# Kernel tuning notes

Hardware: AMD Instinct MI355X
Metric: run time of the kernel (lower is better)

Reference implementation:

```python
import jax, jax.numpy as jnp
import numpy as np

B, T, F, H, S = 32, 2000, 80, 256, 100
CH = [256, 256]
D = 2 * H  # bidirectional output dim


def _conv1d_relu(x, w, b):
    # x: (B,C_in,T), w: (C_out,C_in,3), 'same' padding, eval-mode dropout = identity
    y = jax.lax.conv_general_dilated(x, w, (1,), [(1, 1)], dimension_numbers=("NCH", "OIH", "NCH"))
    return jax.nn.relu(y + b[None, :, None])


def _lstm_dir(x, mask, wih, whh, b):
    # Masked LSTM == packed-sequence semantics: state frozen and output zero past length.
    # PyTorch gate order: i, f, g, o.  x: (B,T,I), mask: (B,T) bool
    Bb = x.shape[0]
    Hh = whh.shape[1]
    h0 = jnp.zeros((Bb, Hh), x.dtype)

    def step(carry, inp):
        h, c = carry
        xt, mt = inp
        g = xt @ wih.T + h @ whh.T + b
        i, f, gg, o = jnp.split(g, 4, axis=-1)
        i = jax.nn.sigmoid(i)
        f = jax.nn.sigmoid(f)
        gg = jnp.tanh(gg)
        o = jax.nn.sigmoid(o)
        cn = f * c + i * gg
        hn = o * jnp.tanh(cn)
        m = mt[:, None]
        return (jnp.where(m, hn, h), jnp.where(m, cn, c)), jnp.where(m, hn, 0.0)

    _, ys = jax.lax.scan(step, (h0, h0), (jnp.swapaxes(x, 0, 1), jnp.swapaxes(mask, 0, 1)))
    return jnp.swapaxes(ys, 0, 1)  # (B,T,H)


def _bilstm_layer(x, mask, lengths, wih, whh, b):
    fwd = _lstm_dir(x, mask, wih[0], whh[0], b[0])
    t = jnp.arange(x.shape[1])[None, :]
    # reverse each sequence within its valid prefix (involution), identity on padding
    rev_idx = jnp.where(t < lengths[:, None], lengths[:, None] - 1 - t, t)
    x_rev = jnp.take_along_axis(x, rev_idx[:, :, None], axis=1)
    bwd = _lstm_dir(x_rev, mask, wih[1], whh[1], b[1])
    bwd = jnp.take_along_axis(bwd, rev_idx[:, :, None], axis=1)
    return jnp.concatenate([fwd, bwd], axis=-1)


def _head(x, w1, b1, w2, b2):
    # Linear -> ReLU -> (Dropout=id) -> Linear(.,1), squeeze last dim
    return (jax.nn.relu(x @ w1.T + b1) @ w2.T + b2)[..., 0]


def _forward(features, feat_lengths, phoneme_segments, seg_lengths,
             conv1_w, conv1_b, conv2_w, conv2_b,
             wih0, whh0, bias0, wih1, whh1, bias1,
             seg_w1, seg_b1, seg_w2, seg_b2,
             utt_w1, utt_b1, utt_w2, utt_b2):
    x = jnp.swapaxes(features, 1, 2)  # (B,F,T)
    x = _conv1d_relu(x, conv1_w, conv1_b)
    x = _conv1d_relu(x, conv2_w, conv2_b)
    x = jnp.swapaxes(x, 1, 2)  # (B,T,C)

    t = jnp.arange(x.shape[1])[None, :]
    mask = t < feat_lengths[:, None]  # (B,T)

    h = _bilstm_layer(x, mask, feat_lengths, wih0, whh0, bias0)
    lstm_out = _bilstm_layer(h, mask, feat_lengths, wih1, whh1, bias1)  # (B,T,2H), zeros at pads

    denom = jnp.maximum(feat_lengths, 1).astype(lstm_out.dtype)[:, None]
    pooled = lstm_out.sum(axis=1) / denom
    utterance_score = _head(pooled, utt_w1, utt_b1, utt_w2, utt_b2)  # (B,)

    # vectorized segment mean-pool (replaces the python double loop)
    s = jnp.clip(phoneme_segments[..., 0], 0, feat_lengths[:, None])
    e = jnp.maximum(s + 1, jnp.minimum(phoneme_segments[..., 1], feat_lengths[:, None]))
    seg_mask = (t[:, None, :] >= s[..., None]) & (t[:, None, :] < e[..., None])  # (B,S,T)
    counts = (e - s).astype(lstm_out.dtype)
    seg_mean = jnp.einsum("bst,btd->bsd", seg_mask.astype(lstm_out.dtype), lstm_out) / counts[..., None]
    scores = _head(seg_mean, seg_w1, seg_b1, seg_w2, seg_b2)  # (B,S)
    valid = jnp.arange(scores.shape[1])[None, :] < seg_lengths[:, None]
    phoneme_scores = jnp.where(valid, scores, 0.0)
    return utterance_score, phoneme_scores


def setup_inputs() -> dict:
    key = jax.random.key(0)
    ks = jax.random.split(key, 24)
    sc = 0.05
    features = jax.random.normal(ks[0], (B, T, F), jnp.float32)
    feat_lengths = jax.random.randint(ks[1], (B,), T // 2, T + 1, dtype=jnp.int32)
    sidx = jnp.arange(S, dtype=jnp.int32)
    starts = (feat_lengths[:, None] * sidx) // S
    ends = (feat_lengths[:, None] * (sidx + 1)) // S
    phoneme_segments = jnp.stack([starts, ends], axis=-1).astype(jnp.int32)  # (B,S,2)
    seg_lengths = jnp.full((B,), S, dtype=jnp.int32)
    return {
        "features": features,
        "feat_lengths": feat_lengths,
        "phoneme_segments": phoneme_segments,
        "seg_lengths": seg_lengths,
        "conv1_w": jax.random.normal(ks[2], (CH[0], F, 3), jnp.float32) * sc,
        "conv1_b": jnp.zeros((CH[0],), jnp.float32),
        "conv2_w": jax.random.normal(ks[3], (CH[1], CH[0], 3), jnp.float32) * sc,
        "conv2_b": jnp.zeros((CH[1],), jnp.float32),
        "wih0": jax.random.normal(ks[4], (2, 4 * H, CH[1]), jnp.float32) * sc,
        "whh0": jax.random.normal(ks[5], (2, 4 * H, H), jnp.float32) * sc,
        "bias0": jnp.zeros((2, 4 * H), jnp.float32),
        "wih1": jax.random.normal(ks[6], (2, 4 * H, 2 * H), jnp.float32) * sc,
        "whh1": jax.random.normal(ks[7], (2, 4 * H, H), jnp.float32) * sc,
        "bias1": jnp.zeros((2, 4 * H), jnp.float32),
        "seg_w1": jax.random.normal(ks[8], (D, D), jnp.float32) * sc,
        "seg_b1": jnp.zeros((D,), jnp.float32),
        "seg_w2": jax.random.normal(ks[9], (1, D), jnp.float32) * sc,
        "seg_b2": jnp.zeros((1,), jnp.float32),
        "utt_w1": jax.random.normal(ks[10], (D, D), jnp.float32) * sc,
        "utt_b1": jnp.zeros((D,), jnp.float32),
        "utt_w2": jax.random.normal(ks[11], (1, D), jnp.float32) * sc,
        "utt_b2": jnp.zeros((1,), jnp.float32),
    }


def reference(features, feat_lengths, phoneme_segments, seg_lengths,
              conv1_w, conv1_b, conv2_w, conv2_b,
              wih0, whh0, bias0, wih1, whh1, bias1,
              seg_w1, seg_b1, seg_w2, seg_b2,
              utt_w1, utt_b1, utt_w2, utt_b2):
    return _forward(features, feat_lengths, phoneme_segments, seg_lengths,
                    conv1_w, conv1_b, conv2_w, conv2_b,
                    wih0, whh0, bias0, wih1, whh1, bias1,
                    seg_w1, seg_b1, seg_w2, seg_b2,
                    utt_w1, utt_b1, utt_w2, utt_b2)
```

## Files before the change

### kernel.cpp

```cpp
#include <hip/hip_runtime.h>
#include <math.h>

#define T_SEQ 2000
#define BATCH 32
#define NSEG  100

typedef unsigned short bf16_t;
typedef unsigned int   u32;
typedef _Float16       half_t;
typedef half_t half2_t __attribute__((ext_vector_type(2)));

#define KP_REG 96
#define KP_LDS 32
#define NG     (KP_LDS / 4)

#define REC_BAR() do {                                         \
    __builtin_amdgcn_sched_barrier(0);                         \
    asm volatile("s_waitcnt lgkmcnt(0)" ::: "memory");         \
    __builtin_amdgcn_s_barrier();                              \
    __builtin_amdgcn_sched_barrier(0);                         \
} while (0)

__device__ __forceinline__ float sigmoidf_(float x) {
    return 1.0f / (1.0f + __expf(-x));
}
__device__ __forceinline__ float tanh_(float x) {
    return 1.0f - 2.0f / (__expf(2.0f * x) + 1.0f);
}
__device__ __forceinline__ float bf2f(bf16_t u) {
    return __uint_as_float((unsigned)u << 16);
}
__device__ __forceinline__ bf16_t f2bf(float f) {
    unsigned x = __float_as_uint(f);
    return (bf16_t)((x + 0x7FFFu + ((x >> 16) & 1u)) >> 16);
}
__device__ __forceinline__ u32 f2h(float f) {
    return (u32)__builtin_bit_cast(unsigned short, (half_t)f);
}
__device__ __forceinline__ float dot2f(u32 w, u32 h, float acc) {
    return __builtin_amdgcn_fdot2(__builtin_bit_cast(half2_t, w),
                                  __builtin_bit_cast(half2_t, h), acc, false);
}
__device__ __forceinline__ u32 rl(u32 v, int l) {
    return (u32)__builtin_amdgcn_readlane((int)v, l);
}

__device__ __forceinline__ float4 ld4(const float* p) { return *(const float4*)p; }
__device__ __forceinline__ float4 ld4(const bf16_t* p) {
    ushort4 u = *(const ushort4*)p;
    return make_float4(bf2f(u.x), bf2f(u.y), bf2f(u.z), bf2f(u.w));
}

__global__ void ws_guard_kernel(float* out, int n) {
    int i = blockIdx.x * blockDim.x + threadIdx.x;
    if (i < n) out[i] = 1e30f;
}

__global__ void transpose3(const float* __restrict__ in, float* __restrict__ out,
                           int D0, int D1, int D2) {
    int i = blockIdx.x * blockDim.x + threadIdx.x;
    int tot = D0 * D1 * D2;
    if (i >= tot) return;
    int d0 = i / (D1 * D2);
    int r  = i - d0 * (D1 * D2);
    int d1 = r / D2;
    int d2 = r - d1 * D2;
    out[(size_t)d0 * D1 * D2 + (size_t)d2 * D1 + d1] = in[i];
}

__global__ __launch_bounds__(256) void pack_whh(const float* __restrict__ whhT,
                                                u32* __restrict__ w16,
                                                u32* __restrict__ wp4) {
    int i = blockIdx.x * 256 + threadIdx.x;
    int d  = i >> 17;
    int r  = i & 131071;
    int kp = r >> 10;
    int j  = r & 1023;
    const float* base = whhT + (size_t)d * 262144;
    u32 lo = f2h(base[(size_t)(2 * kp)     * 1024 + j]);
    u32 hi = f2h(base[(size_t)(2 * kp + 1) * 1024 + j]);
    u32 val = lo | (hi << 16);
    w16[i] = val;
    if (kp >= KP_REG) {
        int g  = (kp - KP_REG) >> 2;
        int cc = (kp - KP_REG) & 3;
        size_t idx = ((((size_t)d * 2 + (j & 1)) * NG + g) * 512 + (j >> 1)) * 4 + cc;
        wp4[idx] = val;
    }
}

template <int MODE, int CIN, typename TA, bool OUT_BF>
__global__ __launch_bounds__(256) void gemm_nt(
    const TA* __restrict__ A, const float* __restrict__ W,
    const float* __restrict__ bias, void* __restrict__ Cout,
    void* __restrict__ Cout2,
    int M, int N, int K, int relu, int t0, int chunkM,
    const int* __restrict__ lens)
{
    __shared__ u32 As[16 * 258];
    __shared__ u32 Ws[16 * 66];
    const int tid    = threadIdx.x;
    const int m_base = blockIdx.x * 256;
    const int n_base = blockIdx.y * 64;
    const int m0     = (tid >> 3) * 8;
    const int n0     = (tid & 7) * 8;
    int zrev = 0;
    if constexpr (MODE == 4) {
        zrev = blockIdx.z;
        if (zrev) { W += (size_t)N * K; bias += N; Cout = Cout2; }
    }
    float acc[8][8] = {};

    for (int k0 = 0; k0 < K; k0 += 32) {
#pragma unroll
        for (int i = 0; i < 8; ++i) {
            int f4  = i * 256 + tid;
            int row = f4 >> 3;
            int k4  = (f4 & 7) << 2;
            int gm  = m_base + row;
            int gk  = k0 + k4;
            float4 v = make_float4(0.f, 0.f, 0.f, 0.f);
            if (gm < M && gk < K) {
                if constexpr (MODE == 1) {
                    int bb  = gm / T_SEQ;
                    int tt  = gm - bb * T_SEQ;
                    int tap = gk / CIN;
                    int cc  = gk - tap * CIN;
                    int ts  = tt + tap - 1;
                    if (ts >= 0 && ts < T_SEQ)
                        v = ld4(A + ((size_t)(bb * T_SEQ + ts) * CIN + cc));
                } else {
                    int bb = gm / chunkM;
                    int r  = gm - bb * chunkM;
                    int t  = zrev ? (lens[bb] - 1 - (t0 + r)) : (t0 + r);
                    if (t >= 0 && t < T_SEQ)
                        v = ld4(A + ((size_t)(bb * T_SEQ + t) * K + gk));
                }
            }
            int kp = k4 >> 1;
            As[(kp + 0) * 258 + row] = f2h(v.x) | (f2h(v.y) << 16);
            As[(kp + 1) * 258 + row] = f2h(v.z) | (f2h(v.w) << 16);
        }
#pragma unroll
        for (int i = 0; i < 2; ++i) {
            int f4  = i * 256 + tid;
            int row = f4 >> 3;
            int k4  = (f4 & 7) << 2;
            int gn  = n_base + row;
            int gk  = k0 + k4;
            float4 v = make_float4(0.f, 0.f, 0.f, 0.f);
            if (gk < K)
                v = *(const float4*)(W + (size_t)gn * K + gk);
            int kp = k4 >> 1;
            Ws[(kp + 0) * 66 + row] = f2h(v.x) | (f2h(v.y) << 16);
            Ws[(kp + 1) * 66 + row] = f2h(v.z) | (f2h(v.w) << 16);
        }
        __syncthreads();
#pragma unroll 8
        for (int kk = 0; kk < 16; ++kk) {
            u32 am[8], wn[8];
#pragma unroll
            for (int j = 0; j < 4; ++j) {
                uint2 a = *(const uint2*)(As + kk * 258 + m0 + 2 * j);
                am[2 * j] = a.x; am[2 * j + 1] = a.y;
                uint2 w = *(const uint2*)(Ws + kk * 66 + n0 + 2 * j);
                wn[2 * j] = w.x; wn[2 * j + 1] = w.y;
            }
#pragma unroll
            for (int im = 0; im < 8; ++im)
#pragma unroll
                for (int in = 0; in < 8; ++in)
                    acc[im][in] = dot2f(am[im], wn[in], acc[im][in]);
        }
        __syncthreads();
    }

    float bs[8];
#pragma unroll
    for (int j = 0; j < 8; ++j) bs[j] = bias[n_base + n0 + j];
#pragma unroll
    for (int im = 0; im < 8; ++im) {
        int gm = m_base + m0 + im;
        if (gm < M) {
            float o[8];
#pragma unroll
            for (int j = 0; j < 8; ++j) {
                float v = acc[im][j] + bs[j];
                o[j] = relu ? fmaxf(v, 0.f) : v;
            }
            if constexpr (OUT_BF) {
                bf16_t* crow = (bf16_t*)Cout + (size_t)gm * N + n_base + n0;
                ushort4 u0 = { f2bf(o[0]), f2bf(o[1]), f2bf(o[2]), f2bf(o[3]) };
                ushort4 u1 = { f2bf(o[4]), f2bf(o[5]), f2bf(o[6]), f2bf(o[7]) };
                *(ushort4*)(crow)     = u0;
                *(ushort4*)(crow + 4) = u1;
            } else {
                float* crow = (float*)Cout + (size_t)gm * N + n_base + n0;
                *(float4*)(crow)     = make_float4(o[0], o[1], o[2], o[3]);
                *(float4*)(crow + 4) = make_float4(o[4], o[5], o[6], o[7]);
            }
        }
    }
}

__global__
__attribute__((amdgpu_flat_work_group_size(512, 512), amdgpu_waves_per_eu(2, 2)))
void rec_fused(
    const float* __restrict__ XpF, const float* __restrict__ XpB,
    const u32* __restrict__ whh16, const uint4* __restrict__ wp4,
    const int* __restrict__ lens,
    float* __restrict__ state, bf16_t* __restrict__ Hout, int s0, int chunk,
    const bf16_t* __restrict__ Ag, const float* __restrict__ Wg2,
    const float* __restrict__ biasg, float* __restrict__ XpFn,
    float* __restrict__ XpBn, int Kg, int t0n)
{
    __shared__ __align__(16) u32 smem[32768 + 1024 + 128];

    const int t = threadIdx.x;

    if (blockIdx.x < 64) {
        uint4* wlds4 = (uint4*)smem;
        float* gs    = (float*)(smem + 32768);
        u32*   hp    = smem + 32768 + 1024;

        const int bd   = blockIdx.x;
        const int b    = bd >> 1;
        const int d    = bd & 1;
        const int j0   = t * 2;
        const int lane = t & 63;
        const int len  = lens[b];
        const int s1   = min(s0 + chunk, len);
        const u32*   Wg = whh16 + (size_t)d * (128 * 1024);
        const uint4* Wp = wp4   + (size_t)d * (2 * NG * 512);

        uint2 w2[KP_REG];
#pragma unroll
        for (int kp = 0; kp < KP_REG; ++kp)
            w2[kp] = *(const uint2*)(Wg + (size_t)kp * 1024 + j0);
#pragma unroll
        for (int i = 0; i < 2 * NG; ++i)
            wlds4[i * 512 + t] = Wp[i * 512 + t];

        float* st = state + bd * 512;
        float c = 0.f, hcur = 0.f;
        if (t < 256) {
            if (s0 > 0) { hcur = st[t]; c = st[256 + t]; }
            u32 hb = f2h(hcur);
            u32 ob = (u32)__shfl_xor((int)hb, 1);
            if (!(t & 1)) hp[t >> 1] = hb | (ob << 16);
        }
        __syncthreads();

        const float* xrow = ((d ? XpB : XpF) + (size_t)b * ((size_t)chunk * 1024));
        const uint4* wpA = wlds4 + t;
        const uint4* wpB = wlds4 + NG * 512 + t;
        for (int s = s0; s < s1; ++s, xrow += 1024) {
            float2 xv = *(const float2*)(xrow + j0);
            uint2 hreg = *(const uint2*)(hp + 2 * lane);
            float a0 = 0.f, a1 = 0.f, b0 = 0.f, b1 = 0.f;
#pragma unroll
            for (int kp = 0; kp < KP_REG; kp += 2) {
                u32 h0 = rl(hreg.x, kp >> 1);
                u32 h1 = rl(hreg.y, kp >> 1);
                a0 = dot2f(w2[kp].x,     h0, a0); a1 = dot2f(w2[kp].y,     h0, a1);
                b0 = dot2f(w2[kp + 1].x, h1, b0); b1 = dot2f(w2[kp + 1].y, h1, b1);
            }
#pragma unroll
            for (int g = 0; g < NG; ++g) {
                uint4 wA = wpA[g * 512];
                uint4 wB = wpB[g * 512];
                const int lb = (KP_REG >> 1) + 2 * g;
                u32 h0 = rl(hreg.x, lb);
                u32 h1 = rl(hreg.y, lb);
                u32 h2 = rl(hreg.x, lb + 1);
                u32 h3 = rl(hreg.y, lb + 1);
                a0 = dot2f(wA.x, h0, a0); a1 = dot2f(wB.x, h0, a1);
                b0 = dot2f(wA.y, h1, b0); b1 = dot2f(wB.y, h1, b1);
                a0 = dot2f(wA.z, h2, a0); a1 = dot2f(wB.z, h2, a1);
                b0 = dot2f(wA.w, h3, b0); b1 = dot2f(wB.w, h3, b1);
            }
            *(float2*)(gs + j0) = make_float2(a0 + b0 + xv.x, a1 + b1 + xv.y);
            REC_BAR();
            if (t < 256) {
                float ig = sigmoidf_(gs[t]);
                float fg = sigmoidf_(gs[256 + t]);
                float gg = tanh_(gs[512 + t]);
                float og = sigmoidf_(gs[768 + t]);
                c = fmaf(fg, c, ig * gg);
                float hn = og * tanh_(c);
                const int tau = d ? (len - 1 - s) : s;
                Hout[(size_t)(b * T_SEQ + tau) * 512 + (d << 8) + t] = f2bf(hn);
                u32 hb = f2h(hn);
                u32 ob = (u32)__shfl_xor((int)hb, 1);
                if (!(t & 1)) hp[t >> 1] = hb | (ob << 16);
                hcur = hn;
            }
            REC_BAR();
        }
        if (t < 256) { st[t] = hcur; st[256 + t] = c; }
        return;
    }

    if (t0n < 0) return;
    const int ngb = gridDim.x - 64;
    const int gb  = blockIdx.x - 64;
    u32* As  = smem;
    u32* Ws0 = smem + 4128;
    u32* Ws1 = smem + 4128 + 1056;
    const int half = t >> 8;
    const int ltid = t & 255;
    u32* Wsh = half ? Ws1 : Ws0;
    const int m0  = (ltid >> 3) * 8;
    const int n0l = (ltid & 7) * 8;
    const int Mc  = 32 * chunk;
    const int gxm = (Mc + 255) >> 8;
    const int U   = gxm * 8 * 2;

    for (int u = gb; u < U; u += ngb) {
        const int dir  = u & 1;
        const int rem  = u >> 1;
        const int mt   = rem >> 3;
        const int np   = rem & 7;
        const int m_base = mt * 256;
        const int n_base = np * 128 + half * 64;
        const float* Wd = Wg2 + (size_t)dir * (1024 * (size_t)Kg);
        const float* bd = biasg + dir * 1024;
        float* Xout = dir ? XpBn : XpFn;
        float acc[8][8] = {};

        for (int k0 = 0; k0 < Kg; k0 += 32) {
#pragma unroll
            for (int i = 0; i < 4; ++i) {
                int f4  = i * 512 + t;
                int row = f4 >> 3;
                int k4  = (f4 & 7) << 2;
                int gm  = m_base + row;
                int gk  = k0 + k4;
                float4 v = make_float4(0.f, 0.f, 0.f, 0.f);
                if (gm < Mc && gk < Kg) {
                    int bb = gm / chunk;
                    int rr = gm - bb * chunk;
                    int tt = dir ? (lens[bb] - 1 - (t0n + rr)) : (t0n + rr);
                    if (tt >= 0 && tt < T_SEQ)
                        v = ld4(Ag + ((size_t)(bb * T_SEQ + tt) * Kg + gk));
                }
                int kp = k4 >> 1;
                As[(kp + 0) * 258 + row] = f2h(v.x) | (f2h(v.y) << 16);
                As[(kp + 1) * 258 + row] = f2h(v.z) | (f2h(v.w) << 16);
            }
#pragma unroll
            for (int i = 0; i < 2; ++i) {
                int f4  = i * 256 + ltid;
                int row = f4 >> 3;
                int k4  = (f4 & 7) << 2;
                int gn  = n_base + row;
                int gk  = k0 + k4;
                float4 v = make_float4(0.f, 0.f, 0.f, 0.f);
                if (gk < Kg)
                    v = *(const float4*)(Wd + (size_t)gn * Kg + gk);
                int kp = k4 >> 1;
                Wsh[(kp + 0) * 66 + row] = f2h(v.x) | (f2h(v.y) << 16);
                Wsh[(kp + 1) * 66 + row] = f2h(v.z) | (f2h(v.w) << 16);
            }
            __syncthreads();
#pragma unroll 8
            for (int kk = 0; kk < 16; ++kk) {
                u32 am[8], wn[8];
#pragma unroll
                for (int j = 0; j < 4; ++j) {
                    uint2 a = *(const uint2*)(As + kk * 258 + m0 + 2 * j);
                    am[2 * j] = a.x; am[2 * j + 1] = a.y;
                    uint2 w = *(const uint2*)(Wsh + kk * 66 + n0l + 2 * j);
                    wn[2 * j] = w.x; wn[2 * j + 1] = w.y;
                }
#pragma unroll
                for (int im = 0; im < 8; ++im)
#pragma unroll
                    for (int in = 0; in < 8; ++in)
                        acc[im][in] = dot2f(am[im], wn[in], acc[im][in]);
            }
            __syncthreads();
        }

        float bs[8];
#pragma unroll
        for (int j = 0; j < 8; ++j) bs[j] = bd[n_base + n0l + j];
#pragma unroll
        for (int im = 0; im < 8; ++im) {
            int gm = m_base + m0 + im;
            if (gm < Mc) {
                float* crow = Xout + (size_t)gm * 1024 + n_base + n0l;
                *(float4*)(crow)     = make_float4(acc[im][0] + bs[0], acc[im][1] + bs[1],
                                                   acc[im][2] + bs[2], acc[im][3] + bs[3]);
                *(float4*)(crow + 4) = make_float4(acc[im][4] + bs[4], acc[im][5] + bs[5],
                                                   acc[im][6] + bs[6], acc[im][7] + bs[7]);
            }
        }
    }
}

__global__ __launch_bounds__(256) void pooled_kernel(
    const bf16_t* __restrict__ L, const int* __restrict__ lens,
    float* __restrict__ pooled)
{
    const int b     = blockIdx.x;
    const int chunk = blockIdx.y;
    const int tid   = threadIdx.x;
    const int len   = lens[b];
    const int t0    = chunk * 250;
    const int t1    = min(t0 + 250, len);
    const float inv = 1.f / fmaxf((float)len, 1.f);
    float s0 = 0.f, s1 = 0.f;
    for (int t = t0; t < t1; ++t) {
        const bf16_t* row = L + (size_t)(b * T_SEQ + t) * 512;
        s0 += bf2f(row[tid]);
        s1 += bf2f(row[tid + 256]);
    }
    if (t1 > t0) {
        atomicAdd(&pooled[b * 512 + tid], s0 * inv);
        atomicAdd(&pooled[b * 512 + 256 + tid], s1 * inv);
    }
}

__global__ __launch_bounds__(256) void utt_head(
    const float* __restrict__ pooled,
    const float* __restrict__ w1T, const float* __restrict__ b1,
    const float* __restrict__ w2, const float* __restrict__ b2,
    float* __restrict__ out)
{
    const int b   = blockIdx.x;
    const int tid = threadIdx.x;
    __shared__ float p[512];
    __shared__ float hid[512];
    __shared__ float red[4];
    p[tid]       = pooled[b * 512 + tid];
    p[tid + 256] = pooled[b * 512 + 256 + tid];
    __syncthreads();
#pragma unroll
    for (int half = 0; half < 2; ++half) {
        int u = tid + half * 256;
        float a = b1[u];
#pragma unroll 8
        for (int k = 0; k < 512; ++k) a = fmaf(w1T[(size_t)k * 512 + u], p[k], a);
        hid[u] = fmaxf(a, 0.f);
    }
    __syncthreads();
    float part = hid[tid] * w2[tid] + hid[tid + 256] * w2[tid + 256];
    for (int off = 32; off; off >>= 1) part += __shfl_down(part, off, 64);
    if ((tid & 63) == 0) red[tid >> 6] = part;
    __syncthreads();
    if (tid == 0) out[b] = red[0] + red[1] + red[2] + red[3] + b2[0];
}

__global__ __launch_bounds__(256) void seg_head(
    const bf16_t* __restrict__ L, const int* __restrict__ lens,
    const int* __restrict__ segs,
    const float* __restrict__ w1T, const float* __restrict__ b1,
    const float* __restrict__ w2, const float* __restrict__ b2,
    const int* __restrict__ seg_lens, float* __restrict__ out)
{
    const int blk = blockIdx.x;
    const int b   = blk / NSEG;
    const int s   = blk - b * NSEG;
    const int tid = threadIdx.x;
    __shared__ float m[512];
    __shared__ float hid[512];
    __shared__ float red[4];
    const int len = lens[b];
    int st = segs[blk * 2 + 0];
    int en = segs[blk * 2 + 1];
    st = min(max(st, 0), len);
    en = max(st + 1, min(en, len));
    const float inv = 1.f / (float)(en - st);
    float a0 = 0.f, a1 = 0.f;
    for (int t = st; t < en; ++t) {
        const bf16_t* row = L + (size_t)(b * T_SEQ + t) * 512;
        a0 += bf2f(row[tid]);
        a1 += bf2f(row[tid + 256]);
    }
    m[tid]       = a0 * inv;
    m[tid + 256] = a1 * inv;
    __syncthreads();
#pragma unroll
    for (int half = 0; half < 2; ++half) {
        int u = tid + half * 256;
        float a = b1[u];
#pragma unroll 8
        for (int k = 0; k < 512; ++k) a = fmaf(w1T[(size_t)k * 512 + u], m[k], a);
        hid[u] = fmaxf(a, 0.f);
    }
    __syncthreads();
    float part = hid[tid] * w2[tid] + hid[tid + 256] * w2[tid + 256];
    for (int off = 32; off; off >>= 1) part += __shfl_down(part, off, 64);
    if ((tid & 63) == 0) red[tid >> 6] = part;
    __syncthreads();
    if (tid == 0)
        out[BATCH + blk] = (s < seg_lens[b]) ? red[0] + red[1] + red[2] + red[3] + b2[0]
                                             : 0.f;
}

extern "C" void kernel_launch(void* const* d_in, const int* in_sizes, int n_in,
                              void* d_out, int out_size, void* d_ws, size_t ws_size,
                              hipStream_t stream)
{
    const float* features = (const float*)d_in[0];
    const int*   feat_len = (const int*)d_in[1];
    const int*   segs     = (const int*)d_in[2];
    const int*   seg_lens = (const int*)d_in[3];
    const float* conv1_w  = (const float*)d_in[4];
    const float* conv1_b  = (const float*)d_in[5];
    const float* conv2_w  = (const float*)d_in[6];
    const float* conv2_b  = (const float*)d_in[7];
    const float* wih0     = (const float*)d_in[8];
    const float* whh0     = (const float*)d_in[9];
    const float* bias0    = (const float*)d_in[10];
    const float* wih1     = (const float*)d_in[11];
    const float* whh1     = (const float*)d_in[12];
    const float* bias1    = (const float*)d_in[13];
    const float* seg_w1   = (const float*)d_in[14];
    const float* seg_b1   = (const float*)d_in[15];
    const float* seg_w2   = (const float*)d_in[16];
    const float* seg_b2   = (const float*)d_in[17];
    const float* utt_w1   = (const float*)d_in[18];
    const float* utt_b1   = (const float*)d_in[19];
    const float* utt_w2   = (const float*)d_in[20];
    const float* utt_b2   = (const float*)d_in[21];
    float* out = (float*)d_out;
    char*  wsb = (char*)d_ws;

    size_t off = 0;
    auto alloc = [&](size_t bytes) -> size_t {
        size_t o = off;
        off += (bytes + 255) & ~(size_t)255;
        return o;
    };
    const size_t o_wt1    = alloc(61440  * 4);
    const size_t o_wt2    = alloc(196608 * 4);
    const size_t o_whh0T  = alloc(524288 * 4);
    const size_t o_whh1T  = alloc(524288 * 4);
    const size_t o_w16_0  = alloc(262144 * 4);
    const size_t o_w16_1  = alloc(262144 * 4);
    const size_t o_wp4_0  = alloc((size_t)2 * 2 * NG * 512 * 16);
    const size_t o_wp4_1  = alloc((size_t)2 * 2 * NG * 512 * 16);
    const size_t o_sw1T   = alloc(262144 * 4);
    const size_t o_uw1T   = alloc(262144 * 4);
    const size_t o_state  = alloc(32768  * 4);
    const size_t o_pooled = alloc(16384  * 4);
    const size_t o_Hcat   = alloc((size_t)32768000 * 2);
    const size_t o_lstm   = alloc((size_t)32768000 * 2);
    const size_t o_y1     = o_lstm;
    const size_t o_x2     = o_lstm + (size_t)16384000 * 2;
    const size_t fixed_end = off;

    const int cands[] = {250, 200, 125, 100, 50, 40, 25, 20, 10};
    int chunk = 0;
    size_t o_Xp[2][2] = {};
    for (int ci = 0; ci < 9; ++ci) {
        int c = cands[ci];
        size_t xp_bytes = ((size_t)c * 32 * 1024 * 4 + 255) & ~(size_t)255;
        if (fixed_end + 4 * xp_bytes <= ws_size) {
            chunk = c;
            o_Xp[0][0] = fixed_end;
            o_Xp[0][1] = fixed_end + xp_bytes;
            o_Xp[1][0] = fixed_end + 2 * xp_bytes;
            o_Xp[1][1] = fixed_end + 3 * xp_bytes;
            break;
        }
    }
    if (chunk == 0) {
        ws_guard_kernel<<<(out_size + 255) / 256, 256, 0, stream>>>(out, out_size);
        return;
    }
    const int nph = T_SEQ / chunk;

    float*  wt1    = (float*)(wsb + o_wt1);
    float*  wt2    = (float*)(wsb + o_wt2);
    float*  whh0T  = (float*)(wsb + o_whh0T);
    float*  whh1T  = (float*)(wsb + o_whh1T);
    u32*    w16_0  = (u32*)(wsb + o_w16_0);
    u32*    w16_1  = (u32*)(wsb + o_w16_1);
    u32*    wp4_0  = (u32*)(wsb + o_wp4_0);
    u32*    wp4_1  = (u32*)(wsb + o_wp4_1);
    float*  sw1T   = (float*)(wsb + o_sw1T);
    float*  uw1T   = (float*)(wsb + o_uw1T);
    float*  state  = (float*)(wsb + o_state);
    float*  pooled = (float*)(wsb + o_pooled);
    bf16_t* Hcat   = (bf16_t*)(wsb + o_Hcat);
    bf16_t* lstm   = (bf16_t*)(wsb + o_lstm);
    bf16_t* y1     = (bf16_t*)(wsb + o_y1);
    bf16_t* x2     = (bf16_t*)(wsb + o_x2);
    float*  XpF[2] = { (float*)(wsb + o_Xp[0][0]), (float*)(wsb + o_Xp[1][0]) };
    float*  XpB[2] = { (float*)(wsb + o_Xp[0][1]), (float*)(wsb + o_Xp[1][1]) };

    hipMemsetAsync(state, 0, 32768 * 4, stream);
    hipMemsetAsync(pooled, 0, 16384 * 4, stream);

    transpose3<<<240, 256, 0, stream>>>(conv1_w, wt1, 256, 80, 3);
    transpose3<<<768, 256, 0, stream>>>(conv2_w, wt2, 256, 256, 3);
    transpose3<<<2048, 256, 0, stream>>>(whh0, whh0T, 2, 1024, 256);
    transpose3<<<2048, 256, 0, stream>>>(whh1, whh1T, 2, 1024, 256);
    transpose3<<<1024, 256, 0, stream>>>(seg_w1, sw1T, 1, 512, 512);
    transpose3<<<1024, 256, 0, stream>>>(utt_w1, uw1T, 1, 512, 512);
    pack_whh<<<1024, 256, 0, stream>>>(whh0T, w16_0, wp4_0);
    pack_whh<<<1024, 256, 0, stream>>>(whh1T, w16_1, wp4_1);

    gemm_nt<1, 80, float, true><<<dim3(250, 4), 256, 0, stream>>>(
        features, wt1, conv1_b, y1, nullptr, 64000, 256, 240, 1, 0, 0, feat_len);
    gemm_nt<1, 256, bf16_t, true><<<dim3(250, 4), 256, 0, stream>>>(
        y1, wt2, conv2_b, x2, nullptr, 64000, 256, 768, 1, 0, 0, feat_len);

    const int gx = (32 * chunk + 255) / 256;
    const int Mc = 32 * chunk;

    gemm_nt<4, 1, bf16_t, false><<<dim3(gx, 16, 2), 256, 0, stream>>>(
        x2, wih0, bias0, XpF[0], XpB[0], Mc, 1024, 256, 0, 0, chunk, feat_len);
    for (int p = 0; p < nph; ++p) {
        const int t0n = (p + 1 < nph) ? (p + 1) * chunk : -1;
        rec_fused<<<256, 512, 0, stream>>>(
            XpF[p & 1], XpB[p & 1], w16_0, (const uint4*)wp4_0, feat_len,
            state, Hcat, p * chunk, chunk,
            x2, wih0, bias0, XpF[(p + 1) & 1], XpB[(p + 1) & 1], 256, t0n);
    }

    hipMemsetAsync(state, 0, 32768 * 4, stream);

    gemm_nt<4, 1, bf16_t, false><<<dim3(gx, 16, 2), 256, 0, stream>>>(
        Hcat, wih1, bias1, XpF[0], XpB[0], Mc, 1024, 512, 0, 0, chunk, feat_len);
    for (int p = 0; p < nph; ++p) {
        const int t0n = (p + 1 < nph) ? (p + 1) * chunk : -1;
        rec_fused<<<256, 512, 0, stream>>>(
            XpF[p & 1], XpB[p & 1], w16_1, (const uint4*)wp4_1, feat_len,
            state, lstm, p * chunk, chunk,
            Hcat, wih1, bias1, XpF[(p + 1) & 1], XpB[(p + 1) & 1], 512, t0n);
    }

    pooled_kernel<<<dim3(32, 8), 256, 0, stream>>>(lstm, feat_len, pooled);
    utt_head<<<32, 256, 0, stream>>>(pooled, uw1T, utt_b1, utt_w2, utt_b2, out);

    seg_head<<<3200, 256, 0, stream>>>(lstm, feat_len, segs, sw1T, seg_b1,
                                       seg_w2, seg_b2, seg_lens, out);
}
```

Measured before the change: 8.667 ms.

## Halve recurrent block to 256 threads, each computing four gate columns

The recurrent LSTM kernel moves from 512 to 256 threads per block, and each thread now produces four gate outputs instead of two. More of W_hh is held in registers (104 of 128 k-pairs), and the rest sits in a repacked LDS layout. This shrinks the per-step barrier and gate-nonlinearity overhead, since every thread is now active in the elementwise phase. The cost is much higher register pressure at one wave per EU, a risk of spills, and half the threads on the overlapped input-projection GEMM blocks, which are reworked to a single 64-wide N tile.

```diff
diff --git a/kernel.cpp b/kernel.cpp
--- a/kernel.cpp
+++ b/kernel.cpp
@@ -10,9 +10,8 @@
 typedef _Float16       half_t;
 typedef half_t half2_t __attribute__((ext_vector_type(2)));
 
-#define KP_REG 96
-#define KP_LDS 32
-#define NG     (KP_LDS / 4)
+#define KP_REG 104
+#define KP_LDS 24
 
 #define REC_BAR() do {                                         \
     __builtin_amdgcn_sched_barrier(0);                         \
@@ -82,9 +81,8 @@
     u32 val = lo | (hi << 16);
     w16[i] = val;
     if (kp >= KP_REG) {
-        int g  = (kp - KP_REG) >> 2;
-        int cc = (kp - KP_REG) & 3;
-        size_t idx = ((((size_t)d * 2 + (j & 1)) * NG + g) * 512 + (j >> 1)) * 4 + cc;
+        int kpl = kp - KP_REG;
+        size_t idx = (((size_t)d * KP_LDS + kpl) * 256 + (j >> 2)) * 4 + (j & 3);
         wp4[idx] = val;
     }
 }
@@ -204,7 +202,7 @@
 }
 
 __global__
-__attribute__((amdgpu_flat_work_group_size(512, 512), amdgpu_waves_per_eu(2, 2)))
+__attribute__((amdgpu_flat_work_group_size(256, 256), amdgpu_waves_per_eu(1, 1)))
 void rec_fused(
     const float* __restrict__ XpF, const float* __restrict__ XpB,
     const u32* __restrict__ whh16, const uint4* __restrict__ wp4,
@@ -214,37 +212,37 @@
     const float* __restrict__ biasg, float* __restrict__ XpFn,
     float* __restrict__ XpBn, int Kg, int t0n)
 {
-    __shared__ __align__(16) u32 smem[32768 + 1024 + 128];
+    __shared__ __align__(16) u32 smem[KP_LDS * 1024 + 1024 + 128];
 
     const int t = threadIdx.x;
 
     if (blockIdx.x < 64) {
         uint4* wlds4 = (uint4*)smem;
-        float* gs    = (float*)(smem + 32768);
-        u32*   hp    = smem + 32768 + 1024;
+        float* gs    = (float*)(smem + KP_LDS * 1024);
+        u32*   hp    = smem + KP_LDS * 1024 + 1024;
 
         const int bd   = blockIdx.x;
         const int b    = bd >> 1;
         const int d    = bd & 1;
-        const int j0   = t * 2;
+        const int j0   = t * 4;
         const int lane = t & 63;
         const int len  = lens[b];
         const int s1   = min(s0 + chunk, len);
         const u32*   Wg = whh16 + (size_t)d * (128 * 1024);
-        const uint4* Wp = wp4   + (size_t)d * (2 * NG * 512);
-
-        uint2 w2[KP_REG];
+        const uint4* Wp = wp4   + (size_t)d * (KP_LDS * 256);
+
+        uint4 w4[KP_REG];
 #pragma unroll
         for (int kp = 0; kp < KP_REG; ++kp)
-            w2[kp] = *(const uint2*)(Wg + (size_t)kp * 1024 + j0);
-#pragma unroll
-        for (int i = 0; i < 2 * NG; ++i)
-            wlds4[i * 512 + t] = Wp[i * 512 + t];
+            w4[kp] = *(const uint4*)(Wg + (size_t)kp * 1024 + j0);
+#pragma unroll
+        for (int i = 0; i < KP_LDS; ++i)
+            wlds4[i * 256 + t] = Wp[i * 256 + t];
 
         float* st = state + bd * 512;
         float c = 0.f, hcur = 0.f;
-        if (t < 256) {
-            if (s0 > 0) { hcur = st[t]; c = st[256 + t]; }
+        if (s0 > 0) { hcur = st[t]; c = st[256 + t]; }
+        {
             u32 hb = f2h(hcur);
             u32 ob = (u32)__shfl_xor((int)hb, 1);
             if (!(t & 1)) hp[t >> 1] = hb | (ob << 16);
@@ -252,36 +250,38 @@
         __syncthreads();
 
         const float* xrow = ((d ? XpB : XpF) + (size_t)b * ((size_t)chunk * 1024));
-        const uint4* wpA = wlds4 + t;
-        const uint4* wpB = wlds4 + NG * 512 + t;
+        const uint4* wpT = wlds4 + t;
         for (int s = s0; s < s1; ++s, xrow += 1024) {
-            float2 xv = *(const float2*)(xrow + j0);
+            float4 xv = *(const float4*)(xrow + j0);
             uint2 hreg = *(const uint2*)(hp + 2 * lane);
-            float a0 = 0.f, a1 = 0.f, b0 = 0.f, b1 = 0.f;
+            float e0 = 0.f, e1 = 0.f, e2 = 0.f, e3 = 0.f;
+            float o0 = 0.f, o1 = 0.f, o2 = 0.f, o3 = 0.f;
 #pragma unroll
             for (int kp = 0; kp < KP_REG; kp += 2) {
                 u32 h0 = rl(hreg.x, kp >> 1);
                 u32 h1 = rl(hreg.y, kp >> 1);
-                a0 = dot2f(w2[kp].x,     h0, a0); a1 = dot2f(w2[kp].y,     h0, a1);
-                b0 = dot2f(w2[kp + 1].x, h1, b0); b1 = dot2f(w2[kp + 1].y, h1, b1);
-            }
-#pragma unroll
-            for (int g = 0; g < NG; ++g) {
-                uint4 wA = wpA[g * 512];
-                uint4 wB = wpB[g * 512];
-                const int lb = (KP_REG >> 1) + 2 * g;
-                u32 h0 = rl(hreg.x, lb);
-                u32 h1 = rl(hreg.y, lb);
-                u32 h2 = rl(hreg.x, lb + 1);
-                u32 h3 = rl(hreg.y, lb + 1);
-                a0 = dot2f(wA.x, h0, a0); a1 = dot2f(wB.x, h0, a1);
-                b0 = dot2f(wA.y, h1, b0); b1 = dot2f(wB.y, h1, b1);
-                a0 = dot2f(wA.z, h2, a0); a1 = dot2f(wB.z, h2, a1);
-                b0 = dot2f(wA.w, h3, b0); b1 = dot2f(wB.w, h3, b1);
-            }
-            *(float2*)(gs + j0) = make_float2(a0 + b0 + xv.x, a1 + b1 + xv.y);
+                uint4 vE = w4[kp], vO = w4[kp + 1];
+                e0 = dot2f(vE.x, h0, e0); e1 = dot2f(vE.y, h0, e1);
+                e2 = dot2f(vE.z, h0, e2); e3 = dot2f(vE.w, h0, e3);
+                o0 = dot2f(vO.x, h1, o0); o1 = dot2f(vO.y, h1, o1);
+                o2 = dot2f(vO.z, h1, o2); o3 = dot2f(vO.w, h1, o3);
+            }
+#pragma unroll
+            for (int kpl = 0; kpl < KP_LDS; kpl += 2) {
+                uint4 vE = wpT[(kpl + 0) * 256];
+                uint4 vO = wpT[(kpl + 1) * 256];
+                const int pi = (KP_REG >> 1) + (kpl >> 1);
+                u32 h0 = rl(hreg.x, pi);
+                u32 h1 = rl(hreg.y, pi);
+                e0 = dot2f(vE.x, h0, e0); e1 = dot2f(vE.y, h0, e1);
+                e2 = dot2f(vE.z, h0, e2); e3 = dot2f(vE.w, h0, e3);
+                o0 = dot2f(vO.x, h1, o0); o1 = dot2f(vO.y, h1, o1);
+                o2 = dot2f(vO.z, h1, o2); o3 = dot2f(vO.w, h1, o3);
+            }
+            *(float4*)(gs + j0) = make_float4(e0 + o0 + xv.x, e1 + o1 + xv.y,
+                                              e2 + o2 + xv.z, e3 + o3 + xv.w);
             REC_BAR();
-            if (t < 256) {
+            {
                 float ig = sigmoidf_(gs[t]);
                 float fg = sigmoidf_(gs[256 + t]);
                 float gg = tanh_(gs[512 + t]);
@@ -297,32 +297,29 @@
             }
             REC_BAR();
         }
-        if (t < 256) { st[t] = hcur; st[256 + t] = c; }
+        st[t] = hcur;
+        st[256 + t] = c;
         return;
     }
 
     if (t0n < 0) return;
     const int ngb = gridDim.x - 64;
     const int gb  = blockIdx.x - 64;
-    u32* As  = smem;
-    u32* Ws0 = smem + 4128;
-    u32* Ws1 = smem + 4128 + 1056;
-    const int half = t >> 8;
-    const int ltid = t & 255;
-    u32* Wsh = half ? Ws1 : Ws0;
-    const int m0  = (ltid >> 3) * 8;
-    const int n0l = (ltid & 7) * 8;
+    u32* As = smem;
+    u32* Ws = smem + 4128;
+    const int m0 = (t >> 3) * 8;
+    const int n0 = (t & 7) * 8;
     const int Mc  = 32 * chunk;
     const int gxm = (Mc + 255) >> 8;
-    const int U   = gxm * 8 * 2;
+    const int U   = gxm * 16 * 2;
 
     for (int u = gb; u < U; u += ngb) {
-        const int dir  = u & 1;
-        const int rem  = u >> 1;
-        const int mt   = rem >> 3;
-        const int np   = rem & 7;
+        const int dir = u & 1;
+        const int rem = u >> 1;
+        const int mt  = rem >> 4;
+        const int nt  = rem & 15;
         const int m_base = mt * 256;
-        const int n_base = np * 128 + half * 64;
+        const int n_base = nt * 64;
         const float* Wd = Wg2 + (size_t)dir * (1024 * (size_t)Kg);
         const float* bd = biasg + dir * 1024;
         float* Xout = dir ? XpBn : XpFn;
@@ -330,8 +327,8 @@
 
         for (int k0 = 0; k0 < Kg; k0 += 32) {
 #pragma unroll
-            for (int i = 0; i < 4; ++i) {
-                int f4  = i * 512 + t;
+            for (int i = 0; i < 8; ++i) {
+                int f4  = i * 256 + t;
                 int row = f4 >> 3;
                 int k4  = (f4 & 7) << 2;
                 int gm  = m_base + row;
@@ -350,7 +347,7 @@
             }
 #pragma unroll
             for (int i = 0; i < 2; ++i) {
-                int f4  = i * 256 + ltid;
+                int f4  = i * 256 + t;
                 int row = f4 >> 3;
                 int k4  = (f4 & 7) << 2;
                 int gn  = n_base + row;
@@ -359,8 +356,8 @@
                 if (gk < Kg)
                     v = *(const float4*)(Wd + (size_t)gn * Kg + gk);
                 int kp = k4 >> 1;
-                Wsh[(kp + 0) * 66 + row] = f2h(v.x) | (f2h(v.y) << 16);
-                Wsh[(kp + 1) * 66 + row] = f2h(v.z) | (f2h(v.w) << 16);
+                Ws[(kp + 0) * 66 + row] = f2h(v.x) | (f2h(v.y) << 16);
+                Ws[(kp + 1) * 66 + row] = f2h(v.z) | (f2h(v.w) << 16);
             }
             __syncthreads();
 #pragma unroll 8
@@ -370,7 +367,7 @@
                 for (int j = 0; j < 4; ++j) {
                     uint2 a = *(const uint2*)(As + kk * 258 + m0 + 2 * j);
                     am[2 * j] = a.x; am[2 * j + 1] = a.y;
-                    uint2 w = *(const uint2*)(Wsh + kk * 66 + n0l + 2 * j);
+                    uint2 w = *(const uint2*)(Ws + kk * 66 + n0 + 2 * j);
                     wn[2 * j] = w.x; wn[2 * j + 1] = w.y;
                 }
 #pragma unroll
@@ -384,12 +381,12 @@
 
         float bs[8];
 #pragma unroll
-        for (int j = 0; j < 8; ++j) bs[j] = bd[n_base + n0l + j];
+        for (int j = 0; j < 8; ++j) bs[j] = bd[n_base + n0 + j];
 #pragma unroll
         for (int im = 0; im < 8; ++im) {
             int gm = m_base + m0 + im;
             if (gm < Mc) {
-                float* crow = Xout + (size_t)gm * 1024 + n_base + n0l;
+                float* crow = Xout + (size_t)gm * 1024 + n_base + n0;
                 *(float4*)(crow)     = make_float4(acc[im][0] + bs[0], acc[im][1] + bs[1],
                                                    acc[im][2] + bs[2], acc[im][3] + bs[3]);
                 *(float4*)(crow + 4) = make_float4(acc[im][4] + bs[4], acc[im][5] + bs[5],
@@ -540,8 +537,8 @@
     const size_t o_whh1T  = alloc(524288 * 4);
     const size_t o_w16_0  = alloc(262144 * 4);
     const size_t o_w16_1  = alloc(262144 * 4);
-    const size_t o_wp4_0  = alloc((size_t)2 * 2 * NG * 512 * 16);
-    const size_t o_wp4_1  = alloc((size_t)2 * 2 * NG * 512 * 16);
+    const size_t o_wp4_0  = alloc((size_t)2 * KP_LDS * 256 * 16);
+    const size_t o_wp4_1  = alloc((size_t)2 * KP_LDS * 256 * 16);
     const size_t o_sw1T   = alloc(262144 * 4);
     const size_t o_uw1T   = alloc(262144 * 4);
     const size_t o_state  = alloc(32768  * 4);
@@ -616,7 +613,7 @@
         x2, wih0, bias0, XpF[0], XpB[0], Mc, 1024, 256, 0, 0, chunk, feat_len);
     for (int p = 0; p < nph; ++p) {
         const int t0n = (p + 1 < nph) ? (p + 1) * chunk : -1;
-        rec_fused<<<256, 512, 0, stream>>>(
+        rec_fused<<<256, 256, 0, stream>>>(
             XpF[p & 1], XpB[p & 1], w16_0, (const uint4*)wp4_0, feat_len,
             state, Hcat, p * chunk, chunk,
             x2, wih0, bias0, XpF[(p + 1) & 1], XpB[(p + 1) & 1], 256, t0n);
@@ -628,7 +625,7 @@
         Hcat, wih1, bias1, XpF[0], XpB[0], Mc, 1024, 512, 0, 0, chunk, feat_len);
     for (int p = 0; p < nph; ++p) {
         const int t0n = (p + 1 < nph) ? (p + 1) * chunk : -1;
-        rec_fused<<<256, 512, 0, stream>>>(
+        rec_fused<<<256, 256, 0, stream>>>(
             XpF[p & 1], XpB[p & 1], w16_1, (const uint4*)wp4_1, feat_len,
             state, lstm, p * chunk, chunk,
             Hcat, wih1, bias1, XpF[(p + 1) & 1], XpB[(p + 1) & 1], 512, t0n);
```

Result: slower. 13.01 ms (+50.1%).
